# Kernel optimization log

Hardware: AMD Instinct MI355X
Metric: run time of the kernel (lower is better)

Reference implementation:

```python
import jax, jax.numpy as jnp
import numpy as np

B, S, D, H = 2, 2048, 1024, 16
DH = D // H


def setup_inputs() -> dict:
    key = jax.random.key(0)
    ks_ = jax.random.split(key, 12)
    s = 1.0 / np.sqrt(D)
    return {
        "qs": jax.random.normal(ks_[0], (B, S, D), jnp.float32),
        "ks": jax.random.normal(ks_[1], (B, S, D), jnp.float32),
        "vs": jax.random.normal(ks_[2], (B, S, D), jnp.float32),
        "mask": jax.random.randint(ks_[3], (B, S), 0, 2) > 0,
        "Wq": jax.random.normal(ks_[4], (D, D), jnp.float32) * s,
        "bq": jnp.zeros((D,), jnp.float32),
        "Wk": jax.random.normal(ks_[5], (D, D), jnp.float32) * s,
        "bk": jnp.zeros((D,), jnp.float32),
        "Wv": jax.random.normal(ks_[6], (D, D), jnp.float32) * s,
        "bv": jnp.zeros((D,), jnp.float32),
        "Wo": jax.random.normal(ks_[7], (D, D), jnp.float32) * s,
        "bo": jnp.zeros((D,), jnp.float32),
    }


def reference(qs, ks, vs, mask, Wq, bq, Wk, bk, Wv, bv, Wo, bo):
    # Linear projections (single-layer MLPs)
    q = qs @ Wq + bq  # [B,S,D]
    k = ks @ Wk + bk
    v = vs @ Wv + bv
    # split heads: B L (H D) -> B H L D
    split = lambda x: x.reshape(B, S, H, DH).transpose(0, 2, 1, 3)
    q, k, v = split(q), split(k), split(v)
    scores = jnp.einsum("bhqd,bhkd->bhqk", q, k) / jnp.sqrt(jnp.float32(DH))
    scores = jnp.where(mask[:, None, None, :], scores, -jnp.inf)
    attn = jax.nn.softmax(scores, axis=-1)  # [B,H,Q,K]
    ctx = jnp.einsum("bhqk,bhkd->bhqd", attn, v)
    ctx = ctx.transpose(0, 2, 1, 3).reshape(B, S, D)  # B H L D -> B L (H D)
    out = ctx @ Wo + bo
    return (out, attn)
```

## Files before the change

kernel.cpp:

```cpp
#include <hip/hip_runtime.h>
#include <hip/hip_bf16.h>
#include <cstdint>

#define NBATCH 2
#define NS 2048
#define NDIM 1024
#define NHEAD 16
#define NDH 64
#define NBH 32

typedef __bf16 bf16x8 __attribute__((ext_vector_type(8)));
typedef float f32x4 __attribute__((ext_vector_type(4)));

#define QK_EXP2_SCALE 0.1803368801111244f

#define WAITV(N) asm volatile("s_waitcnt vmcnt(" #N ")" ::: "memory")
#define FENCE asm volatile("" ::: "memory")

#define EXP2(x) __builtin_amdgcn_exp2f(x)

static __device__ __forceinline__ f32x4 mfma16(bf16x8 a, bf16x8 b, f32x4 c) {
  return __builtin_amdgcn_mfma_f32_16x16x32_bf16(a, b, c, 0, 0, 0);
}

static __device__ __forceinline__ void gload_lds16(const void* g, void* l) {
  __builtin_amdgcn_global_load_lds(
      (const __attribute__((address_space(1))) uint32_t*)g,
      (__attribute__((address_space(3))) uint32_t*)l, 16, 0, 0);
}

__global__ __launch_bounds__(256) void k_cvt_x(const float* __restrict__ q,
                                               const float* __restrict__ k,
                                               const float* __restrict__ v,
                                               __bf16* __restrict__ out) {
  const float* src = blockIdx.y == 0 ? q : (blockIdx.y == 1 ? k : v);
  __bf16* dst = out + (size_t)blockIdx.y * (size_t)(4096 * 1024);
  int i = blockIdx.x * 256 + threadIdx.x;
  const float4* s4 = reinterpret_cast<const float4*>(src) + (size_t)i * 2;
  float4 a = s4[0], b = s4[1];
  bf16x8 o;
  o[0] = (__bf16)a.x; o[1] = (__bf16)a.y; o[2] = (__bf16)a.z; o[3] = (__bf16)a.w;
  o[4] = (__bf16)b.x; o[5] = (__bf16)b.y; o[6] = (__bf16)b.z; o[7] = (__bf16)b.w;
  *reinterpret_cast<bf16x8*>(dst + (size_t)i * 8) = o;
}

__global__ __launch_bounds__(256) void k_cvt_w(const float* __restrict__ Wq,
                                               const float* __restrict__ Wk,
                                               const float* __restrict__ Wv,
                                               const float* __restrict__ Wo,
                                               __bf16* __restrict__ out,
                                               const int* __restrict__ mask,
                                               float* __restrict__ biasf) {
  if (blockIdx.y == 4) {
    int t = blockIdx.x * 256 + threadIdx.x;
    if (t < NBATCH * NS) biasf[t] = mask[t] ? 0.f : -1e30f;
    return;
  }
  const float* W = blockIdx.y == 0 ? Wq : (blockIdx.y == 1 ? Wk
                   : (blockIdx.y == 2 ? Wv : Wo));
  __bf16* dst = out + (size_t)blockIdx.y * (size_t)(1024 * 1024);
  int t = blockIdx.x * 256 + threadIdx.x;
  int n = t & 1023;
  int kc = t >> 10;
  bf16x8 o;
#pragma unroll
  for (int j = 0; j < 8; ++j) o[j] = (__bf16)W[(size_t)(kc * 8 + j) * 1024 + n];
  *reinterpret_cast<bf16x8*>(dst + (size_t)n * 1024 + kc * 8) = o;
}

__global__ __launch_bounds__(256) void k_tr_v(const __bf16* __restrict__ V,
                                              __bf16* __restrict__ Vt) {
  int t = blockIdx.x * 256 + threadIdx.x;
  int d = t & 63;
  int sc = (t >> 6) & 255;
  int bh = t >> 14;
  bf16x8 o;
#pragma unroll
  for (int j = 0; j < 8; ++j)
    o[j] = V[((size_t)bh * 2048 + sc * 8 + j) * 64 + d];
  *reinterpret_cast<bf16x8*>(Vt + ((size_t)bh * 64 + d) * 2048 + sc * 8) = o;
}

__global__ __launch_bounds__(256) void k_gemm(const __bf16* __restrict__ Abase,
                                              const __bf16* __restrict__ Btbase,
                                              const float* __restrict__ b0,
                                              const float* __restrict__ b1,
                                              const float* __restrict__ b2,
                                              void* __restrict__ outbase,
                                              int mode) {
  __shared__ __align__(16) char smem[65536];
  const int job = blockIdx.y;
  const __bf16* A = Abase + (size_t)job * (size_t)(4096 * 1024);
  const __bf16* Bt = Btbase + (size_t)job * (size_t)(1024 * 1024);
  const float* bias = job == 0 ? b0 : (job == 1 ? b1 : b2);
  const int x = blockIdx.x;
  const int mt = (x & 7) * 4 + (x >> 6);
  const int nt = (x >> 3) & 7;
  const int tid = threadIdx.x;
  const int w = tid >> 6, l = tid & 63;
  const int wr = w >> 1, wc = w & 1;

  auto stage = [&](int buf, int kt) {
    const int k0 = kt * 64;
    char* al = smem + buf * 32768;
    char* bl = al + 16384;
#pragma unroll
    for (int i = 0; i < 4; ++i) {
      int ch = tid + i * 256;
      int r = ch >> 3, c = ch & 7;
      int cs = c ^ (r & 7);
      gload_lds16(A + (size_t)(mt * 128 + r) * 1024 + k0 + cs * 8, al + ch * 16);
      gload_lds16(Bt + (size_t)(nt * 128 + r) * 1024 + k0 + cs * 8, bl + ch * 16);
    }
  };

  f32x4 acc[4][4] = {};
  stage(0, 0);
  for (int kt = 0; kt < 16; ++kt) {
    __syncthreads();
    if (kt + 1 < 16) stage((kt + 1) & 1, kt + 1);
    const char* al = smem + (kt & 1) * 32768;
    const char* bl = al + 16384;
#pragma unroll
    for (int ks = 0; ks < 2; ++ks) {
      bf16x8 af[4], bfr[4];
#pragma unroll
      for (int i = 0; i < 4; ++i) {
        int ra = wr * 64 + i * 16 + (l & 15);
        int ca = (ks * 4 + (l >> 4)) ^ (ra & 7);
        af[i] = *reinterpret_cast<const bf16x8*>(al + ra * 128 + ca * 16);
        int rb = wc * 64 + i * 16 + (l & 15);
        int cb = (ks * 4 + (l >> 4)) ^ (rb & 7);
        bfr[i] = *reinterpret_cast<const bf16x8*>(bl + rb * 128 + cb * 16);
      }
#pragma unroll
      for (int mi = 0; mi < 4; ++mi)
#pragma unroll
        for (int ni = 0; ni < 4; ++ni)
          acc[mi][ni] = mfma16(af[mi], bfr[ni], acc[mi][ni]);
    }
  }

  if (mode == 0) {
    const float sc = (job == 0) ? QK_EXP2_SCALE : 1.0f;
    __bf16* outp = (__bf16*)outbase + (size_t)job * (size_t)(NBH * NS * NDH);
#pragma unroll
    for (int mi = 0; mi < 4; ++mi)
#pragma unroll
      for (int ni = 0; ni < 4; ++ni)
#pragma unroll
        for (int r = 0; r < 4; ++r) {
          int m = mt * 128 + wr * 64 + mi * 16 + (l >> 4) * 4 + r;
          int n = nt * 128 + wc * 64 + ni * 16 + (l & 15);
          float v = (acc[mi][ni][r] + bias[n]) * sc;
          int b = m >> 11, s = m & 2047, h = n >> 6, d = n & 63;
          outp[(((size_t)(b * 16 + h)) * 2048 + s) * 64 + d] = (__bf16)v;
        }
  } else {
    float* outp = (float*)outbase;
#pragma unroll
    for (int mi = 0; mi < 4; ++mi)
#pragma unroll
      for (int ni = 0; ni < 4; ++ni)
#pragma unroll
        for (int r = 0; r < 4; ++r) {
          int m = mt * 128 + wr * 64 + mi * 16 + (l >> 4) * 4 + r;
          int n = nt * 128 + wc * 64 + ni * 16 + (l & 15);
          __builtin_nontemporal_store(acc[mi][ni][r] + bias[n],
                                      outp + (size_t)m * 1024 + n);
        }
  }
}

__global__ __launch_bounds__(256, 2) void k_attn(
    const __bf16* __restrict__ Qw, const __bf16* __restrict__ Kw,
    const __bf16* __restrict__ Vt, const float* __restrict__ biasf,
    float* __restrict__ attn_out, __bf16* __restrict__ ctx_out) {
  __shared__ __align__(16) char smem[75264];
  const int wg = blockIdx.x;
  const int swz = (wg & 7) * 64 + (wg >> 3);
  const int qt = swz & 15;
  const int bh = swz >> 4;
  const int b = bh >> 4;
  const int tid = threadIdx.x, w = tid >> 6, l = tid & 63;
  const int g = l >> 4, c = l & 15;
  const int qw = qt * 128 + w * 32;
  const float* biasb = biasf + b * 2048;

  bf16x8 qa[2][2];
#pragma unroll
  for (int mi = 0; mi < 2; ++mi)
#pragma unroll
    for (int ks = 0; ks < 2; ++ks)
      qa[mi][ks] = *reinterpret_cast<const bf16x8*>(
          Qw + ((size_t)bh * 2048 + qw + mi * 16 + c) * 64 + ks * 32 + g * 8);

  auto stageK = [&](char* dst, int kt) {
#pragma unroll
    for (int i = 0; i < 4; ++i) {
      int ch = tid + i * 256;
      int r = ch >> 3, cc = ch & 7;
      int cs = cc ^ (r & 7);
      gload_lds16(Kw + ((size_t)bh * 2048 + kt * 128 + r) * 64 + cs * 8,
                  dst + ch * 16);
    }
  };
  auto stageV = [&](char* dst, int kt) {
#pragma unroll
    for (int i = 0; i < 4; ++i) {
      int ch = tid + i * 256;
      int r = ch >> 4, cc = ch & 15;
      int cs = cc ^ (r & 15);
      gload_lds16(Vt + ((size_t)bh * 64 + r) * 2048 + kt * 128 + cs * 8,
                  dst + ch * 16);
    }
  };
  auto stageBias = [&](int slot, int kt) {
    if (l < 32)
      gload_lds16(biasb + kt * 128 + l * 4, smem + 73728 + slot * 512);
  };

  float rs[2] = {0.f, 0.f};
  stageK(smem, 0);
  stageBias(0, 0);
  int sl = 0;
  for (int kt = 0; kt < 16; ++kt) {
    int nx = (sl + 1 == 3) ? 0 : sl + 1;
    if (kt + 1 < 16) {
      stageK(smem + nx * 16384, kt + 1);
      stageBias(nx, kt + 1);
      WAITV(5);
    } else {
      WAITV(0);
    }
    __builtin_amdgcn_s_barrier();
    FENCE;
    const char* kl = smem + sl * 16384;
    const float* bl = (const float*)(smem + 73728 + sl * 512);
#pragma unroll
    for (int nb = 0; nb < 8; ++nb) {
      bf16x8 kb[2];
#pragma unroll
      for (int ks = 0; ks < 2; ++ks) {
        int r = nb * 16 + c;
        int cc = (ks * 4 + g) ^ (r & 7);
        kb[ks] = *reinterpret_cast<const bf16x8*>(kl + r * 128 + cc * 16);
      }
      f32x4 cinit = *reinterpret_cast<const f32x4*>(bl + nb * 16 + g * 4);
#pragma unroll
      for (int mi = 0; mi < 2; ++mi) {
        f32x4 s = mfma16(kb[0], qa[mi][0], cinit);
        s = mfma16(kb[1], qa[mi][1], s);
        rs[mi] += EXP2(s[0]) + EXP2(s[1]) + EXP2(s[2]) + EXP2(s[3]);
      }
    }
    sl = nx;
  }
  float inv_[2];
#pragma unroll
  for (int mi = 0; mi < 2; ++mi) {
    float v = rs[mi];
    v += __shfl_xor(v, 16, 64);
    v += __shfl_xor(v, 32, 64);
    inv_[mi] = v > 0.f ? 1.f / v : 0.f;
  }
  FENCE; __builtin_amdgcn_s_barrier(); FENCE;

  f32x4 ctx[2][4] = {};
  float* attnb = attn_out + (size_t)bh * 2048 * 2048;
  char* pF = smem + 65536 + w * 2048;
  stageK(smem, 0);
  stageV(smem + 32768, 0);
  stageBias(0, 0);
  for (int kt = 0; kt < 16; ++kt) {
    if (kt + 1 < 16) {
      int nx3 = (kt + 1) % 3;
      stageK(smem + ((kt + 1) & 1) * 16384, kt + 1);
      stageV(smem + 32768 + ((kt + 1) & 1) * 16384, kt + 1);
      stageBias(nx3, kt + 1);
    }
    if (kt == 0) WAITV(9);
    else if (kt == 15) WAITV(16);
    else WAITV(25);
    FENCE; __builtin_amdgcn_s_barrier(); FENCE;
    const char* kl = smem + (kt & 1) * 16384;
    const char* vl = smem + 32768 + (kt & 1) * 16384;
    const float* bl = (const float*)(smem + 73728 + (kt % 3) * 512);
#pragma unroll
    for (int kc = 0; kc < 4; ++kc) {
      bf16x8 kbj[2][2];
      f32x4 cin[2];
#pragma unroll
      for (int j = 0; j < 2; ++j) {
        const int nb = kc * 2 + j;
#pragma unroll
        for (int ks = 0; ks < 2; ++ks) {
          int r = nb * 16 + c;
          int cc = (ks * 4 + g) ^ (r & 7);
          kbj[j][ks] = *reinterpret_cast<const bf16x8*>(kl + r * 128 + cc * 16);
        }
        cin[j] = *reinterpret_cast<const f32x4*>(bl + nb * 16 + g * 4);
      }
      bf16x8 vb[4];
#pragma unroll
      for (int nd = 0; nd < 4; ++nd) {
        int dd = nd * 16 + c;
        int ch = (kc * 4 + g) ^ (dd & 15);
        vb[nd] = *reinterpret_cast<const bf16x8*>(vl + dd * 256 + ch * 16);
      }
#pragma unroll
      for (int mi = 0; mi < 2; ++mi) {
#pragma unroll
        for (int j = 0; j < 2; ++j) {
          f32x4 s = mfma16(kbj[j][0], qa[mi][0], cin[j]);
          s = mfma16(kbj[j][1], qa[mi][1], s);
          f32x4 p;
#pragma unroll
          for (int r = 0; r < 4; ++r) p[r] = EXP2(s[r]) * inv_[mi];
          *reinterpret_cast<f32x4*>(
              pF + c * 128 + (((j * 4 + g) ^ (c & 7)) * 16)) = p;
        }
        bf16x8 pa;
        {
          f32x4 lo = *reinterpret_cast<const f32x4*>(
              pF + c * 128 + (((2 * g) ^ (c & 7)) * 16));
          f32x4 hi = *reinterpret_cast<const f32x4*>(
              pF + c * 128 + (((2 * g + 1) ^ (c & 7)) * 16));
          pa[0] = (__bf16)lo[0]; pa[1] = (__bf16)lo[1];
          pa[2] = (__bf16)lo[2]; pa[3] = (__bf16)lo[3];
          pa[4] = (__bf16)hi[0]; pa[5] = (__bf16)hi[1];
          pa[6] = (__bf16)hi[2]; pa[7] = (__bf16)hi[3];
        }
#pragma unroll
        for (int nd = 0; nd < 4; ++nd)
          ctx[mi][nd] = mfma16(pa, vb[nd], ctx[mi][nd]);
#pragma unroll
        for (int u = 0; u < 2; ++u) {
          int rr = u * 8 + (l >> 3);
          int ch = (l & 7) ^ (rr & 7);
          f32x4 pv = *reinterpret_cast<const f32x4*>(pF + rr * 128 + ch * 16);
          __builtin_nontemporal_store(
              pv, reinterpret_cast<f32x4*>(
                      attnb + (size_t)(qw + mi * 16 + rr) * 2048 + kt * 128 +
                      kc * 32 + (l & 7) * 4));
        }
      }
    }
    FENCE; __builtin_amdgcn_s_barrier(); FENCE;
  }

  const int h = bh & 15;
#pragma unroll
  for (int mi = 0; mi < 2; ++mi)
#pragma unroll
    for (int nd = 0; nd < 4; ++nd)
#pragma unroll
      for (int r = 0; r < 4; ++r) {
        int m = b * 2048 + qw + mi * 16 + g * 4 + r;
        int n = h * 64 + nd * 16 + c;
        ctx_out[(size_t)m * 1024 + n] = (__bf16)ctx[mi][nd][r];
      }
}

extern "C" void kernel_launch(void* const* d_in, const int* in_sizes, int n_in,
                              void* d_out, int out_size, void* d_ws,
                              size_t ws_size, hipStream_t stream) {
  const float* qs = (const float*)d_in[0];
  const float* ks = (const float*)d_in[1];
  const float* vs = (const float*)d_in[2];
  const int* mask = (const int*)d_in[3];
  const float* Wq = (const float*)d_in[4];
  const float* bq = (const float*)d_in[5];
  const float* Wk = (const float*)d_in[6];
  const float* bk = (const float*)d_in[7];
  const float* Wv = (const float*)d_in[8];
  const float* bv = (const float*)d_in[9];
  const float* Wo = (const float*)d_in[10];
  const float* bo = (const float*)d_in[11];

  char* ws = (char*)d_ws;
  __bf16* Xb = (__bf16*)(ws);
  __bf16* Wt = (__bf16*)(ws + 25165824);
  __bf16* QKV = (__bf16*)(ws + 58720256);
  float* biasf = (float*)(ws + 83886080);
  __bf16* Vt = (__bf16*)(ws);
  __bf16* ctx = (__bf16*)(ws + 8388608);
  float* out = (float*)d_out;
  float* attn = out + (size_t)4194304;

  k_cvt_x<<<dim3(2048, 3), 256, 0, stream>>>(qs, ks, vs, Xb);
  k_cvt_w<<<dim3(512, 5), 256, 0, stream>>>(Wq, Wk, Wv, Wo, Wt, mask, biasf);
  k_gemm<<<dim3(256, 3), 256, 0, stream>>>(Xb, Wt, bq, bk, bv, QKV, 0);
  k_tr_v<<<dim3(2048), 256, 0, stream>>>(QKV + (size_t)2 * 4194304, Vt);
  k_attn<<<dim3(512), 256, 0, stream>>>(QKV, QKV + (size_t)4194304, Vt, biasf,
                                        attn, ctx);
  k_gemm<<<dim3(256, 1), 256, 0, stream>>>(ctx, Wt + (size_t)3 * 1048576, bo,
                                           bo, bo, d_out, 1);
}
```

Before: 211.3 us.

## Split attention row-sum pass into separate high-occupancy kernel

Moves the first pass of the two-pass softmax (row sums of exp scores) out of the attention kernel into a new k_rowsum kernel. That kernel uses less LDS and launch bounds allowing four blocks per CU, and writes inverse row sums to a workspace buffer. The attention kernel then reads those sums and runs only the P and PV pass. This adds a kernel launch and a small global round trip, and the row-sum pass now uses a simpler double-buffered pipeline with a full wait each iteration.

```diff
diff --git a/kernel.cpp b/kernel.cpp
--- a/kernel.cpp
+++ b/kernel.cpp
@@ -172,10 +172,88 @@
   }
 }
 
-__global__ __launch_bounds__(256, 2) void k_attn(
+__global__ __launch_bounds__(256, 4) void k_rowsum(
+    const __bf16* __restrict__ Qw, const __bf16* __restrict__ Kw,
+    const float* __restrict__ biasf, float* __restrict__ invb) {
+  __shared__ __align__(16) char smem[33792];
+  const int wg = blockIdx.x;
+  const int swz = (wg & 7) * 64 + (wg >> 3);
+  const int qt = swz & 15;
+  const int bh = swz >> 4;
+  const int b = bh >> 4;
+  const int tid = threadIdx.x, w = tid >> 6, l = tid & 63;
+  const int g = l >> 4, c = l & 15;
+  const int qw = qt * 128 + w * 32;
+  const float* biasb = biasf + b * 2048;
+
+  bf16x8 qa[2][2];
+#pragma unroll
+  for (int mi = 0; mi < 2; ++mi)
+#pragma unroll
+    for (int ks = 0; ks < 2; ++ks)
+      qa[mi][ks] = *reinterpret_cast<const bf16x8*>(
+          Qw + ((size_t)bh * 2048 + qw + mi * 16 + c) * 64 + ks * 32 + g * 8);
+
+  auto stageK = [&](char* dst, int kt) {
+#pragma unroll
+    for (int i = 0; i < 4; ++i) {
+      int ch = tid + i * 256;
+      int r = ch >> 3, cc = ch & 7;
+      int cs = cc ^ (r & 7);
+      gload_lds16(Kw + ((size_t)bh * 2048 + kt * 128 + r) * 64 + cs * 8,
+                  dst + ch * 16);
+    }
+  };
+  auto stageBias = [&](int slot, int kt) {
+    if (l < 32)
+      gload_lds16(biasb + kt * 128 + l * 4, smem + 32768 + slot * 512);
+  };
+
+  float rs[2] = {0.f, 0.f};
+  stageK(smem, 0);
+  stageBias(0, 0);
+  for (int kt = 0; kt < 16; ++kt) {
+    WAITV(0);
+    FENCE; __builtin_amdgcn_s_barrier(); FENCE;
+    if (kt + 1 < 16) {
+      stageK(smem + ((kt + 1) & 1) * 16384, kt + 1);
+      stageBias((kt + 1) & 1, kt + 1);
+    }
+    const char* kl = smem + (kt & 1) * 16384;
+    const float* bl = (const float*)(smem + 32768 + (kt & 1) * 512);
+#pragma unroll
+    for (int nb = 0; nb < 8; ++nb) {
+      bf16x8 kb[2];
+#pragma unroll
+      for (int ks = 0; ks < 2; ++ks) {
+        int r = nb * 16 + c;
+        int cc = (ks * 4 + g) ^ (r & 7);
+        kb[ks] = *reinterpret_cast<const bf16x8*>(kl + r * 128 + cc * 16);
+      }
+      f32x4 cinit = *reinterpret_cast<const f32x4*>(bl + nb * 16 + g * 4);
+#pragma unroll
+      for (int mi = 0; mi < 2; ++mi) {
+        f32x4 s = mfma16(kb[0], qa[mi][0], cinit);
+        s = mfma16(kb[1], qa[mi][1], s);
+        rs[mi] += EXP2(s[0]) + EXP2(s[1]) + EXP2(s[2]) + EXP2(s[3]);
+      }
+    }
+  }
+#pragma unroll
+  for (int mi = 0; mi < 2; ++mi) {
+    float v = rs[mi];
+    v += __shfl_xor(v, 16, 64);
+    v += __shfl_xor(v, 32, 64);
+    if (g == 0)
+      invb[(size_t)bh * 2048 + qw + mi * 16 + c] = v > 0.f ? 1.f / v : 0.f;
+  }
+}
+
+__global__ __launch_bounds__(256, 2) void k_attn2(
     const __bf16* __restrict__ Qw, const __bf16* __restrict__ Kw,
     const __bf16* __restrict__ Vt, const float* __restrict__ biasf,
-    float* __restrict__ attn_out, __bf16* __restrict__ ctx_out) {
+    const float* __restrict__ invb, float* __restrict__ attn_out,
+    __bf16* __restrict__ ctx_out) {
   __shared__ __align__(16) char smem[75264];
   const int wg = blockIdx.x;
   const int swz = (wg & 7) * 64 + (wg >> 3);
@@ -187,6 +265,10 @@
   const int qw = qt * 128 + w * 32;
   const float* biasb = biasf + b * 2048;
 
+  float inv_[2];
+  inv_[0] = invb[(size_t)bh * 2048 + qw + c];
+  inv_[1] = invb[(size_t)bh * 2048 + qw + 16 + c];
+
   bf16x8 qa[2][2];
 #pragma unroll
   for (int mi = 0; mi < 2; ++mi)
@@ -194,6 +276,7 @@
     for (int ks = 0; ks < 2; ++ks)
       qa[mi][ks] = *reinterpret_cast<const bf16x8*>(
           Qw + ((size_t)bh * 2048 + qw + mi * 16 + c) * 64 + ks * 32 + g * 8);
+  asm volatile("s_waitcnt vmcnt(0)" ::: "memory");
 
   auto stageK = [&](char* dst, int kt) {
 #pragma unroll
@@ -219,52 +302,6 @@
     if (l < 32)
       gload_lds16(biasb + kt * 128 + l * 4, smem + 73728 + slot * 512);
   };
-
-  float rs[2] = {0.f, 0.f};
-  stageK(smem, 0);
-  stageBias(0, 0);
-  int sl = 0;
-  for (int kt = 0; kt < 16; ++kt) {
-    int nx = (sl + 1 == 3) ? 0 : sl + 1;
-    if (kt + 1 < 16) {
-      stageK(smem + nx * 16384, kt + 1);
-      stageBias(nx, kt + 1);
-      WAITV(5);
-    } else {
-      WAITV(0);
-    }
-    __builtin_amdgcn_s_barrier();
-    FENCE;
-    const char* kl = smem + sl * 16384;
-    const float* bl = (const float*)(smem + 73728 + sl * 512);
-#pragma unroll
-    for (int nb = 0; nb < 8; ++nb) {
-      bf16x8 kb[2];
-#pragma unroll
-      for (int ks = 0; ks < 2; ++ks) {
-        int r = nb * 16 + c;
-        int cc = (ks * 4 + g) ^ (r & 7);
-        kb[ks] = *reinterpret_cast<const bf16x8*>(kl + r * 128 + cc * 16);
-      }
-      f32x4 cinit = *reinterpret_cast<const f32x4*>(bl + nb * 16 + g * 4);
-#pragma unroll
-      for (int mi = 0; mi < 2; ++mi) {
-        f32x4 s = mfma16(kb[0], qa[mi][0], cinit);
-        s = mfma16(kb[1], qa[mi][1], s);
-        rs[mi] += EXP2(s[0]) + EXP2(s[1]) + EXP2(s[2]) + EXP2(s[3]);
-      }
-    }
-    sl = nx;
-  }
-  float inv_[2];
-#pragma unroll
-  for (int mi = 0; mi < 2; ++mi) {
-    float v = rs[mi];
-    v += __shfl_xor(v, 16, 64);
-    v += __shfl_xor(v, 32, 64);
-    inv_[mi] = v > 0.f ? 1.f / v : 0.f;
-  }
-  FENCE; __builtin_amdgcn_s_barrier(); FENCE;
 
   f32x4 ctx[2][4] = {};
   float* attnb = attn_out + (size_t)bh * 2048 * 2048;
@@ -383,6 +420,7 @@
   __bf16* Wt = (__bf16*)(ws + 25165824);
   __bf16* QKV = (__bf16*)(ws + 58720256);
   float* biasf = (float*)(ws + 83886080);
+  float* invb = (float*)(ws + 83902464);
   __bf16* Vt = (__bf16*)(ws);
   __bf16* ctx = (__bf16*)(ws + 8388608);
   float* out = (float*)d_out;
@@ -392,8 +430,10 @@
   k_cvt_w<<<dim3(512, 5), 256, 0, stream>>>(Wq, Wk, Wv, Wo, Wt, mask, biasf);
   k_gemm<<<dim3(256, 3), 256, 0, stream>>>(Xb, Wt, bq, bk, bv, QKV, 0);
   k_tr_v<<<dim3(2048), 256, 0, stream>>>(QKV + (size_t)2 * 4194304, Vt);
-  k_attn<<<dim3(512), 256, 0, stream>>>(QKV, QKV + (size_t)4194304, Vt, biasf,
-                                        attn, ctx);
+  k_rowsum<<<dim3(512), 256, 0, stream>>>(QKV, QKV + (size_t)4194304, biasf,
+                                          invb);
+  k_attn2<<<dim3(512), 256, 0, stream>>>(QKV, QKV + (size_t)4194304, Vt,
+                                         biasf, invb, attn, ctx);
   k_gemm<<<dim3(256, 1), 256, 0, stream>>>(ctx, Wt + (size_t)3 * 1048576, bo,
                                            bo, bo, d_out, 1);
 }
```

After: 219.1 us. +3.7%, slower.
